# Kernel optimization log

Hardware: AMD Instinct MI355X
Metric: run time of the kernel (lower is better)

## Reference

```python
import jax, jax.numpy as jnp
import numpy as np

B, N, IN, OUT, H = 8, 256, 256, 256, 4
HD = OUT // H  # 64
ALPHA = 0.2    # LeakyReLU negative slope
EPS = 1e-5


def layernorm(x, g, b):
    m = x.mean(-1, keepdims=True)
    v = jnp.mean(jnp.square(x - m), axis=-1, keepdims=True)
    return (x - m) / jnp.sqrt(v + EPS) * g + b


def setup_inputs() -> dict:
    key = jax.random.key(0)
    ks = jax.random.split(key, 16)
    s = 0.05
    return {
        'h':    jax.random.normal(ks[0], (B, N, IN), jnp.float32),
        'adj':  jax.random.randint(ks[1], (B, N, N), 0, 2, jnp.int32),
        # per-head params (leading dim H)
        'W':    jax.random.normal(ks[2], (H, IN, HD), jnp.float32) * s,      # node proj (no bias)
        'We1':  jax.random.normal(ks[3], (H, 2 * IN, HD), jnp.float32) * s,  # edge_encoder lin
        'be1':  jnp.zeros((H, HD), jnp.float32),
        'Wa1':  jax.random.normal(ks[4], (H, 3 * HD, HD), jnp.float32) * s,  # attn mlp lin1
        'ba1':  jnp.zeros((H, HD), jnp.float32),
        'wa2':  jax.random.normal(ks[5], (H, HD), jnp.float32) * s,          # attn mlp lin2 -> scalar
        'ba2':  jnp.zeros((H,), jnp.float32),
        'ln_g': jnp.ones((H, HD), jnp.float32),   # per-head LayerNorm
        'ln_b': jnp.zeros((H, HD), jnp.float32),
        'Wo':   jax.random.normal(ks[6], (OUT, OUT), jnp.float32) * s,       # output projection
        'bo':   jnp.zeros((OUT,), jnp.float32),
        'ln2_g': jnp.ones((OUT,), jnp.float32),   # final LayerNorm
        'ln2_b': jnp.zeros((OUT,), jnp.float32),
    }


def _head(h, adj_mask, W, We1, be1, Wa1, ba1, wa2, ba2, g, b):
    # h: [B,N,IN]; adj_mask: [B,N,N] bool (True where adj==0)
    Wh = jnp.einsum('bnf,fd->bnd', h, W)                      # [B,N,HD]
    # attention MLP lin1 applied to concat([Wh_i, Wh_j, edge]):
    # split weight so the per-node parts are computed once, broadcast over pairs
    Wa, Wb, We = Wa1[:HD], Wa1[HD:2 * HD], Wa1[2 * HD:]
    si = jnp.einsum('bnd,de->bne', Wh, Wa) + ba1              # [B,N,HD]
    sj = jnp.einsum('bnd,de->bne', Wh, Wb)                    # [B,N,HD]
    # edge encoder: Linear(cat[h_i,h_j]) -> leaky_relu, split likewise
    ei = jnp.einsum('bnf,fd->bnd', h, We1[:IN]) + be1         # [B,N,HD]
    ej = jnp.einsum('bnf,fd->bnd', h, We1[IN:])               # [B,N,HD]
    edge = jax.nn.leaky_relu(ei[:, :, None, :] + ej[:, None, :, :], ALPHA)  # [B,N,N,HD]
    hidden = jax.nn.leaky_relu(
        si[:, :, None, :] + sj[:, None, :, :] + jnp.einsum('bijd,de->bije', edge, We),
        ALPHA)                                                # [B,N,N,HD]
    e = jnp.einsum('bijd,d->bij', hidden, wa2) + ba2          # [B,N,N]
    e = jnp.where(adj_mask, -1e9, e)
    attn = jax.nn.softmax(e, axis=-1)                         # [B,N,N]
    hp = jnp.einsum('bij,bjd->bid', attn, Wh)                 # [B,N,HD]
    return layernorm(hp, g, b)


def reference(h, adj, W, We1, be1, Wa1, ba1, wa2, ba2, ln_g, ln_b, Wo, bo, ln2_g, ln2_b):
    adj_mask = (adj == 0)
    heads = [
        _head(h, adj_mask, W[i], We1[i], be1[i], Wa1[i], ba1[i],
              wa2[i], ba2[i], ln_g[i], ln_b[i])
        for i in range(H)
    ]
    concat = jnp.concatenate(heads, axis=-1)                  # [B,N,OUT]
    out = jnp.einsum('bnf,fo->bno', concat, Wo) + bo
    out = out + h                                             # residual (IN == OUT)
    return layernorm(out, ln2_g, ln2_b)
```

## Files before the change

### kernel.cpp

```cpp
#include <hip/hip_runtime.h>
#include <hip/hip_bf16.h>

#define B_ 8
#define N_ 256
#define IN_ 256
#define OUT_ 256
#define H_ 4
#define HD_ 64
#define ALPHA_ 0.2f
#define EPS_ 1e-5f

#define S_ (B_*H_*N_*HD_)


typedef unsigned short ushort_t;
typedef __attribute__((ext_vector_type(8))) short short8;
typedef __attribute__((ext_vector_type(4))) float floatx4;

__device__ __forceinline__ float lrelu(float x) { return fmaxf(x, ALPHA_ * x); }
__device__ __forceinline__ ushort_t f2b(float x) {
    unsigned u = __float_as_uint(x);
    unsigned r = ((u >> 16) & 1u) + 0x7fffu;
    return (ushort_t)((u + r) >> 16);
}
__device__ __forceinline__ unsigned pk2(float x0, float x1) {
    __hip_bfloat162 p = __float22bfloat162_rn(make_float2(x0, x1));
    return *(unsigned*)&p;
}

__global__ __launch_bounds__(256) void setup_kernel(
    const float* __restrict__ h, const float* __restrict__ W,
    const float* __restrict__ We1, const float* __restrict__ Wa1,
    const float* __restrict__ Wo,
    ushort_t* __restrict__ h_b, ushort_t* __restrict__ wfull,
    ushort_t* __restrict__ wo_t, ushort_t* __restrict__ bw_b)
{
    const int blk = blockIdx.x;
    if (blk < 512) {
        const int i = (blk * 256 + threadIdx.x) * 4;
        float4 v = *(const float4*)&h[i];
        uint2 o; o.x = pk2(v.x, v.y); o.y = pk2(v.z, v.w);
        *(uint2*)&h_b[i] = o;
    } else if (blk < 1536) {
        const int bb = blk - 512;
        const int hh = bb >> 8, f = bb & 255;
        const int c = threadIdx.x;
        __shared__ float Wlds[64];
        if (c < 64) Wlds[c] = W[(size_t)(hh * 256 + f) * 64 + c];
        __syncthreads();
        float v;
        if (c < 64)       v = Wlds[c];
        else if (c < 128) v = We1[(size_t)(hh * 512 + f) * 64 + (c - 64)];
        else if (c < 192) v = We1[(size_t)(hh * 512 + 256 + f) * 64 + (c - 128)];
        else {
            float s = 0.f;
            const float* wa = Wa1 + (size_t)hh * 192 * 64 + (c - 192);
            #pragma unroll 4
            for (int g = 0; g < 64; ++g) s += Wlds[g] * wa[(size_t)g * 64];
            v = s;
        }
        wfull[(size_t)(hh * 256 + c) * 256 + f] = f2b(v);
    } else if (blk < 1552) {
        const int bb = blk - 1536;
        const int to = bb & 3, tf = bb >> 2;
        const int r0 = threadIdx.x >> 6, cc = threadIdx.x & 63;
        __shared__ float t[64][65];
        for (int rr = r0; rr < 64; rr += 4)
            t[rr][cc] = Wo[(size_t)(tf * 64 + rr) * 256 + to * 64 + cc];
        __syncthreads();
        for (int rr = r0; rr < 64; rr += 4)
            wo_t[(size_t)(to * 64 + rr) * 256 + tf * 64 + cc] = f2b(t[cc][rr]);
    } else {
        const int hh = blk - 1552;
        for (int idx = threadIdx.x; idx < 64 * 128; idx += 256) {
            const int e = idx >> 7, k = idx & 127;
            const int row = (k < 64) ? (128 + k) : k;
            bw_b[hh * 8192 + idx] = f2b(Wa1[(size_t)hh * 192 * 64 + row * 64 + e]);
        }
    }
}

__global__ __launch_bounds__(256) void prep2_kernel(
    const ushort_t* __restrict__ h_b, const ushort_t* __restrict__ wfull,
    const float* __restrict__ be1, const float* __restrict__ ba1,
    float* __restrict__ ws)
{
    const int gm = blockIdx.x & 63, gn = blockIdx.x >> 6;
    const int tid = threadIdx.x, lane = tid & 63, wid = tid >> 6;
    const int quad = lane >> 4, l15 = lane & 15;

    float*    ei_f = ws;
    float*    si_f = ws + S_;
    ushort_t* ej_b = (ushort_t*)(ws + 2 * (size_t)S_);
    ushort_t* Wh_b = ej_b + S_;
    ushort_t* WhT_b = (ushort_t*)(ws + 4 * (size_t)S_) + 262144 + 65536 + 32768;

    floatx4 acc[2][2];
    #pragma unroll
    for (int mt = 0; mt < 2; ++mt)
        #pragma unroll
        for (int nt = 0; nt < 2; ++nt) acc[mt][nt] = (floatx4){0.f,0.f,0.f,0.f};

    #pragma unroll 2
    for (int ks = 0; ks < 8; ++ks) {
        short8 afr[2], bfr[2];
        #pragma unroll
        for (int mt = 0; mt < 2; ++mt)
            afr[mt] = *(const short8*)&h_b[(size_t)(gm * 32 + mt * 16 + l15) * 256 + ks * 32 + quad * 8];
        #pragma unroll
        for (int nt = 0; nt < 2; ++nt)
            bfr[nt] = *(const short8*)&wfull[(size_t)(gn * 128 + wid * 32 + nt * 16 + l15) * 256 + ks * 32 + quad * 8];
        #pragma unroll
        for (int mt = 0; mt < 2; ++mt)
            #pragma unroll
            for (int nt = 0; nt < 2; ++nt)
                acc[mt][nt] = __builtin_amdgcn_mfma_f32_16x16x32_bf16(afr[mt], bfr[nt], acc[mt][nt], 0, 0, 0);
    }

    #pragma unroll
    for (int nt = 0; nt < 2; ++nt) {
        const int colg = gn * 128 + wid * 32 + nt * 16 + l15;
        const int head = colg >> 8, c = colg & 255, type = c >> 6, d = c & 63;
        #pragma unroll
        for (int mt = 0; mt < 2; ++mt)
            #pragma unroll
            for (int reg = 0; reg < 4; ++reg) {
                const int row = gm * 32 + mt * 16 + quad * 4 + reg;
                const int b = row >> 8, n = row & 255;
                const size_t idx = ((size_t)(b * H_ + head) * 256 + n) * 64 + d;
                const float v = acc[mt][nt][reg];
                if (type == 0) {
                    const ushort_t vb = f2b(v);
                    Wh_b[idx] = vb;
                    WhT_b[((size_t)(b * H_ + head) * 64 + d) * 256 + n] = vb;
                }
                else if (type == 1) ei_f[idx] = v + be1[head * 64 + d];
                else if (type == 2) ej_b[idx] = f2b(v);
                else                si_f[idx] = v + ba1[head * 64 + d];
            }
    }
}

__global__ __launch_bounds__(256, 2) void attn_kernel(
    const int* __restrict__ adj, const float* __restrict__ wa2,
    const float* __restrict__ ba2, const float* __restrict__ ln_g,
    const float* __restrict__ ln_b, float* __restrict__ ws)
{
    const int blk  = blockIdx.x;
    const int ig   = blk & 15;
    const int head = (blk >> 4) & 3;
    const int b    = blk >> 6;
    const int i0   = ig * 16;
    const int tid  = threadIdx.x;
    const int lane = tid & 63;
    const int wid  = tid >> 6;
    const int quad = lane >> 4;
    const int l15  = lane & 15;
    const int bh   = b * H_ + head;

    __shared__ float    P_s[16 * 256];
    __shared__ ushort_t Pb_s[16 * 264];
    __shared__ float    ei_s[16 * 64];
    __shared__ float    si_s[16 * 64];
    __shared__ unsigned long long adjm_s[16 * 4];
    __shared__ float    hp_s[16 * 68];

    const float*    ei_f = ws;
    const float*    si_f = ws + S_;
    const ushort_t* ej_b = (const ushort_t*)(ws + 2 * (size_t)S_);
    const ushort_t* Wh_b = ej_b + S_;
    ushort_t*       conc = (ushort_t*)(ws + 3 * (size_t)S_) + 524288;
    const ushort_t* bw_b = (const ushort_t*)(ws + 4 * (size_t)S_) + 262144 + 65536;
    const ushort_t* WhT_b = bw_b + 32768;

    {
        const int ii = tid >> 4, c = tid & 15;
        *(float4*)&ei_s[ii * 64 + c * 4] =
            *(const float4*)&ei_f[((size_t)(bh * 256 + i0 + ii)) * 64 + c * 4];
        *(float4*)&si_s[ii * 64 + c * 4] =
            *(const float4*)&si_f[((size_t)(bh * 256 + i0 + ii)) * 64 + c * 4];
    }
    {
        int av[16];
        #pragma unroll
        for (int r = 0; r < 16; ++r)
            av[r] = adj[((size_t)(b * 256 + i0 + r)) * 256 + tid];
        #pragma unroll
        for (int r = 0; r < 16; ++r) {
            unsigned long long mk = __ballot(av[r] != 0);
            if (lane == 0) adjm_s[r * 4 + wid] = mk;
        }
    }

    uint4  ejr[4][2];
    short8 bfrWe[4][2];
    floatx4 sjacc[4][4];
    #pragma unroll
    for (int mt = 0; mt < 4; ++mt) {
        const size_t jrow = (size_t)(bh * 256 + wid * 64 + mt * 16 + l15) * 64;
        #pragma unroll
        for (int kk = 0; kk < 2; ++kk)
            ejr[mt][kk] = *(const uint4*)&ej_b[jrow + kk * 32 + quad * 8];
    }
    #pragma unroll
    for (int nt = 0; nt < 4; ++nt)
        #pragma unroll
        for (int ks = 0; ks < 2; ++ks)
            bfrWe[nt][ks] = *(const short8*)&bw_b[head * 8192 + (nt * 16 + l15) * 128 + ks * 32 + quad * 8];
    {
        #pragma unroll
        for (int mt = 0; mt < 4; ++mt)
            #pragma unroll
            for (int nt = 0; nt < 4; ++nt) sjacc[mt][nt] = (floatx4){0.f,0.f,0.f,0.f};
        #pragma unroll
        for (int ks = 2; ks < 4; ++ks) {
            short8 whf[4], bfrWb[4];
            #pragma unroll
            for (int mt = 0; mt < 4; ++mt)
                whf[mt] = *(const short8*)&Wh_b[((size_t)(bh * 256 + wid * 64 + mt * 16 + l15)) * 64
                                                + (ks - 2) * 32 + quad * 8];
            #pragma unroll
            for (int nt = 0; nt < 4; ++nt)
                bfrWb[nt] = *(const short8*)&bw_b[head * 8192 + (nt * 16 + l15) * 128 + ks * 32 + quad * 8];
            #pragma unroll
            for (int mt = 0; mt < 4; ++mt)
                #pragma unroll
                for (int nt = 0; nt < 4; ++nt)
                    sjacc[mt][nt] = __builtin_amdgcn_mfma_f32_16x16x32_bf16(
                        whf[mt], bfrWb[nt], sjacc[mt][nt], 0, 0, 0);
        }
    }

    float wv[4];
    #pragma unroll
    for (int nt = 0; nt < 4; ++nt) wv[nt] = wa2[head * 64 + nt * 16 + l15];
    const float ba2h = ba2[head];

    __syncthreads();

    for (int i = 0; i < 16; ++i) {
        floatx4 acc[4][4];
        #pragma unroll
        for (int mt = 0; mt < 4; ++mt)
            #pragma unroll
            for (int nt = 0; nt < 4; ++nt) acc[mt][nt] = sjacc[mt][nt];

        #pragma unroll
        for (int ks = 0; ks < 2; ++ks) {
            short8 afr[4];
            float ev[8];
            *(float4*)&ev[0] = *(const float4*)&ei_s[i * 64 + ks * 32 + quad * 8];
            *(float4*)&ev[4] = *(const float4*)&ei_s[i * 64 + ks * 32 + quad * 8 + 4];
            #pragma unroll
            for (int mt = 0; mt < 4; ++mt) {
                const unsigned* rw = (const unsigned*)&ejr[mt][ks];
                union { unsigned u[4]; short8 s; } ow;
                #pragma unroll
                for (int p = 0; p < 4; ++p) {
                    float x0 = __uint_as_float(rw[p] << 16)         + ev[2 * p];
                    float x1 = __uint_as_float(rw[p] & 0xffff0000u) + ev[2 * p + 1];
                    ow.u[p] = pk2(lrelu(x0), lrelu(x1));
                }
                afr[mt] = ow.s;
            }
            #pragma unroll
            for (int mt = 0; mt < 4; ++mt)
                #pragma unroll
                for (int nt = 0; nt < 4; ++nt)
                    acc[mt][nt] = __builtin_amdgcn_mfma_f32_16x16x32_bf16(
                        afr[mt], bfrWe[nt][ks], acc[mt][nt], 0, 0, 0);
        }

        float sv[4];
        #pragma unroll
        for (int nt = 0; nt < 4; ++nt) sv[nt] = si_s[i * 64 + nt * 16 + l15];
        #pragma unroll
        for (int mt = 0; mt < 4; ++mt) {
            #pragma unroll
            for (int reg = 0; reg < 4; ++reg) {
                float val = 0.f;
                #pragma unroll
                for (int nt = 0; nt < 4; ++nt)
                    val += lrelu(acc[mt][nt][reg] + sv[nt]) * wv[nt];
                val += __shfl_xor(val, 1, 64);
                val += __shfl_xor(val, 2, 64);
                val += __shfl_xor(val, 4, 64);
                val += __shfl_xor(val, 8, 64);
                if (l15 == 0)
                    P_s[i * 256 + wid * 64 + mt * 16 + quad * 4 + reg] = val + ba2h;
            }
        }
    }
    __syncthreads();

    #pragma unroll
    for (int rr = 0; rr < 4; ++rr) {
        const int r = rr * 4 + wid;
        float4 v = *(const float4*)&P_s[r * 256 + lane * 4];
        const unsigned mk = (unsigned)(adjm_s[r * 4 + quad] >> (l15 * 4)) & 0xFu;
        float v0 = (mk & 1u) ? v.x : -1e9f;
        float v1 = (mk & 2u) ? v.y : -1e9f;
        float v2 = (mk & 4u) ? v.z : -1e9f;
        float v3 = (mk & 8u) ? v.w : -1e9f;
        float m = fmaxf(fmaxf(v0, v1), fmaxf(v2, v3));
        #pragma unroll
        for (int off = 32; off >= 1; off >>= 1) m = fmaxf(m, __shfl_xor(m, off, 64));
        float p0 = __expf(v0 - m), p1 = __expf(v1 - m);
        float p2 = __expf(v2 - m), p3 = __expf(v3 - m);
        float s = (p0 + p1) + (p2 + p3);
        #pragma unroll
        for (int off = 32; off >= 1; off >>= 1) s += __shfl_xor(s, off, 64);
        const float inv = 1.f / s;
        uint2 o; o.x = pk2(p0 * inv, p1 * inv); o.y = pk2(p2 * inv, p3 * inv);
        *(uint2*)&Pb_s[r * 264 + lane * 4] = o;
    }
    __syncthreads();

    floatx4 hacc = (floatx4){0.f,0.f,0.f,0.f};
    #pragma unroll
    for (int s = 0; s < 8; ++s) {
        short8 af = *(const short8*)&Pb_s[l15 * 264 + s * 32 + quad * 8];
        short8 bf = *(const short8*)&WhT_b[((size_t)(bh * 64) + wid * 16 + l15) * 256 + s * 32 + quad * 8];
        hacc = __builtin_amdgcn_mfma_f32_16x16x32_bf16(af, bf, hacc, 0, 0, 0);
    }
    #pragma unroll
    for (int reg = 0; reg < 4; ++reg)
        hp_s[(quad * 4 + reg) * 68 + wid * 16 + l15] = hacc[reg];
    __syncthreads();

    const float gg = ln_g[head * 64 + lane];
    const float bb = ln_b[head * 64 + lane];
    #pragma unroll
    for (int pss = 0; pss < 4; ++pss) {
        const int r = pss * 4 + wid;
        const float v = hp_s[r * 68 + lane];
        float s1 = v, s2 = v * v;
        #pragma unroll
        for (int off = 32; off >= 1; off >>= 1) {
            s1 += __shfl_xor(s1, off, 64);
            s2 += __shfl_xor(s2, off, 64);
        }
        const float mean = s1 * (1.f / 64.f);
        const float var = s2 * (1.f / 64.f) - mean * mean;
        const float o = (v - mean) * __frsqrt_rn(var + EPS_) * gg + bb;
        conc[((size_t)(b * 256 + i0 + r)) * 256 + head * 64 + lane] = f2b(o);
    }
}

__global__ __launch_bounds__(256) void out2_kernel(
    const float* __restrict__ h, const float* __restrict__ bo,
    const float* __restrict__ ln2_g, const float* __restrict__ ln2_b,
    const ushort_t* __restrict__ conc, const ushort_t* __restrict__ wo_t,
    float* __restrict__ out)
{
    const int rowbase = blockIdx.x * 16;
    const int tid = threadIdx.x, lane = tid & 63, wid = tid >> 6;
    const int quad = lane >> 4, l15 = lane & 15;

    __shared__ float s1a[16][4], s2a[16][4];

    floatx4 acc[4];
    #pragma unroll
    for (int nt = 0; nt < 4; ++nt) acc[nt] = (floatx4){0.f,0.f,0.f,0.f};

    #pragma unroll 2
    for (int ks = 0; ks < 8; ++ks) {
        short8 afr = *(const short8*)&conc[(size_t)(rowbase + l15) * 256 + ks * 32 + quad * 8];
        #pragma unroll
        for (int nt = 0; nt < 4; ++nt) {
            short8 bfr = *(const short8*)&wo_t[(size_t)(wid * 64 + nt * 16 + l15) * 256 + ks * 32 + quad * 8];
            acc[nt] = __builtin_amdgcn_mfma_f32_16x16x32_bf16(afr, bfr, acc[nt], 0, 0, 0);
        }
    }

    float x[4][4], s1[4], s2[4];
    #pragma unroll
    for (int reg = 0; reg < 4; ++reg) { s1[reg] = 0.f; s2[reg] = 0.f; }
    #pragma unroll
    for (int nt = 0; nt < 4; ++nt) {
        const int col = wid * 64 + nt * 16 + l15;
        const float bv = bo[col];
        #pragma unroll
        for (int reg = 0; reg < 4; ++reg) {
            const int row = rowbase + quad * 4 + reg;
            float v = acc[nt][reg] + bv + h[(size_t)row * 256 + col];
            x[nt][reg] = v;
            s1[reg] += v;
            s2[reg] += v * v;
        }
    }
    #pragma unroll
    for (int reg = 0; reg < 4; ++reg) {
        #pragma unroll
        for (int off = 1; off <= 8; off <<= 1) {
            s1[reg] += __shfl_xor(s1[reg], off, 64);
            s2[reg] += __shfl_xor(s2[reg], off, 64);
        }
        if (l15 == 0) {
            s1a[quad * 4 + reg][wid] = s1[reg];
            s2a[quad * 4 + reg][wid] = s2[reg];
        }
    }
    __syncthreads();

    #pragma unroll
    for (int reg = 0; reg < 4; ++reg) {
        const int r = quad * 4 + reg;
        const float S1 = s1a[r][0] + s1a[r][1] + s1a[r][2] + s1a[r][3];
        const float S2 = s2a[r][0] + s2a[r][1] + s2a[r][2] + s2a[r][3];
        const float mean = S1 * (1.f / 256.f);
        const float var = S2 * (1.f / 256.f) - mean * mean;
        const float rs = __frsqrt_rn(var + EPS_);
        const int row = rowbase + r;
        #pragma unroll
        for (int nt = 0; nt < 4; ++nt) {
            const int col = wid * 64 + nt * 16 + l15;
            out[(size_t)row * 256 + col] =
                (x[nt][reg] - mean) * rs * ln2_g[col] + ln2_b[col];
        }
    }
}

extern "C" void kernel_launch(void* const* d_in, const int* in_sizes, int n_in,
                              void* d_out, int out_size, void* d_ws, size_t ws_size,
                              hipStream_t stream)
{
    const float* h    = (const float*)d_in[0];
    const int*   adj  = (const int*)  d_in[1];
    const float* W    = (const float*)d_in[2];
    const float* We1  = (const float*)d_in[3];
    const float* be1  = (const float*)d_in[4];
    const float* Wa1  = (const float*)d_in[5];
    const float* ba1  = (const float*)d_in[6];
    const float* wa2  = (const float*)d_in[7];
    const float* ba2  = (const float*)d_in[8];
    const float* ln_g = (const float*)d_in[9];
    const float* ln_b = (const float*)d_in[10];
    const float* Wo   = (const float*)d_in[11];
    const float* bo   = (const float*)d_in[12];
    const float* ln2g = (const float*)d_in[13];
    const float* ln2b = (const float*)d_in[14];

    float* ws = (float*)d_ws;
    ushort_t* h_b   = (ushort_t*)(ws + 3 * (size_t)S_);
    ushort_t* conc  = h_b + 524288;
    ushort_t* wfull = (ushort_t*)(ws + 4 * (size_t)S_);
    ushort_t* wo_t  = wfull + 262144;
    ushort_t* bw_b  = wo_t + 65536;
    float* out = (float*)d_out;

    setup_kernel<<<1556, 256, 0, stream>>>(h, W, We1, Wa1, Wo, h_b, wfull, wo_t, bw_b);
    prep2_kernel<<<512,  256, 0, stream>>>(h_b, wfull, be1, ba1, ws);
    attn_kernel <<<512,  256, 0, stream>>>(adj, wa2, ba2, ln_g, ln_b, ws);
    out2_kernel <<<B_ * 16, 256, 0, stream>>>(h, bo, ln2g, ln2b, conc, wo_t, out);
}
```

Measured before the change: 187.8 us.

## Fuse h bf16 conversion into projection GEMM and restructure weight build kernel

The separate h-to-bf16 conversion pass is dropped; the projection GEMM now loads fp32 h directly and packs it to bf16 in registers. The weight-building kernel is reorganised from 1556 small blocks into 36 blocks that stage 64x64 tiles in shared memory, giving coalesced transposed writes to wfull. This removes one global round trip of h and many tiny blocks. In exchange, each GEMM block reads twice the bytes for the A operand and repeats the conversion, and the weight build runs on far fewer blocks.

```diff
diff --git a/kernel.cpp b/kernel.cpp
--- a/kernel.cpp
+++ b/kernel.cpp
@@ -28,42 +28,53 @@
     return *(unsigned*)&p;
 }
 
-__global__ __launch_bounds__(256) void setup_kernel(
-    const float* __restrict__ h, const float* __restrict__ W,
-    const float* __restrict__ We1, const float* __restrict__ Wa1,
-    const float* __restrict__ Wo,
-    ushort_t* __restrict__ h_b, ushort_t* __restrict__ wfull,
-    ushort_t* __restrict__ wo_t, ushort_t* __restrict__ bw_b)
+__global__ __launch_bounds__(256) void build_kernel(
+    const float* __restrict__ W, const float* __restrict__ We1,
+    const float* __restrict__ Wa1, const float* __restrict__ Wo,
+    ushort_t* __restrict__ wfull, ushort_t* __restrict__ wo_t,
+    ushort_t* __restrict__ bw_b)
 {
     const int blk = blockIdx.x;
-    if (blk < 512) {
-        const int i = (blk * 256 + threadIdx.x) * 4;
-        float4 v = *(const float4*)&h[i];
-        uint2 o; o.x = pk2(v.x, v.y); o.y = pk2(v.z, v.w);
-        *(uint2*)&h_b[i] = o;
-    } else if (blk < 1536) {
-        const int bb = blk - 512;
-        const int hh = bb >> 8, f = bb & 255;
-        const int c = threadIdx.x;
-        __shared__ float Wlds[64];
-        if (c < 64) Wlds[c] = W[(size_t)(hh * 256 + f) * 64 + c];
-        __syncthreads();
-        float v;
-        if (c < 64)       v = Wlds[c];
-        else if (c < 128) v = We1[(size_t)(hh * 512 + f) * 64 + (c - 64)];
-        else if (c < 192) v = We1[(size_t)(hh * 512 + 256 + f) * 64 + (c - 128)];
-        else {
-            float s = 0.f;
-            const float* wa = Wa1 + (size_t)hh * 192 * 64 + (c - 192);
-            #pragma unroll 4
-            for (int g = 0; g < 64; ++g) s += Wlds[g] * wa[(size_t)g * 64];
-            v = s;
-        }
-        wfull[(size_t)(hh * 256 + c) * 256 + f] = f2b(v);
-    } else if (blk < 1552) {
-        const int bb = blk - 1536;
+    const int tid = threadIdx.x;
+    if (blk < 16) {
+        const int hh = blk >> 2, cq = blk & 3;
+        __shared__ float tl[64][65];
+        __shared__ float wa_l[64][65];
+        const int r4 = tid >> 6;
+        const int cl = tid & 63;
+        if (cq == 3) {
+            for (int g = r4; g < 64; g += 4)
+                wa_l[g][cl] = Wa1[((size_t)hh * 192 + g) * 64 + cl];
+            __syncthreads();
+        }
+        for (int ft = 0; ft < 4; ++ft) {
+            const int f0 = ft * 64;
+            if (cq < 3) {
+                for (int r = r4; r < 64; r += 4) {
+                    float v;
+                    if (cq == 0)      v = W  [((size_t)hh * 256 + f0 + r) * 64 + cl];
+                    else if (cq == 1) v = We1[((size_t)hh * 512 + f0 + r) * 64 + cl];
+                    else              v = We1[((size_t)hh * 512 + 256 + f0 + r) * 64 + cl];
+                    tl[r][cl] = v;
+                }
+            } else {
+                for (int f = r4; f < 64; f += 4) {
+                    float acc = 0.f;
+                    const float* wrow = &W[((size_t)hh * 256 + f0 + f) * 64];
+                    #pragma unroll 8
+                    for (int g = 0; g < 64; ++g) acc += wrow[g] * wa_l[g][cl];
+                    tl[f][cl] = acc;
+                }
+            }
+            __syncthreads();
+            for (int cr = r4; cr < 64; cr += 4)
+                wfull[((size_t)hh * 256 + cq * 64 + cr) * 256 + f0 + cl] = f2b(tl[cl][cr]);
+            __syncthreads();
+        }
+    } else if (blk < 32) {
+        const int bb = blk - 16;
         const int to = bb & 3, tf = bb >> 2;
-        const int r0 = threadIdx.x >> 6, cc = threadIdx.x & 63;
+        const int r0 = tid >> 6, cc = tid & 63;
         __shared__ float t[64][65];
         for (int rr = r0; rr < 64; rr += 4)
             t[rr][cc] = Wo[(size_t)(tf * 64 + rr) * 256 + to * 64 + cc];
@@ -71,8 +82,8 @@
         for (int rr = r0; rr < 64; rr += 4)
             wo_t[(size_t)(to * 64 + rr) * 256 + tf * 64 + cc] = f2b(t[cc][rr]);
     } else {
-        const int hh = blk - 1552;
-        for (int idx = threadIdx.x; idx < 64 * 128; idx += 256) {
+        const int hh = blk - 32;
+        for (int idx = tid; idx < 64 * 128; idx += 256) {
             const int e = idx >> 7, k = idx & 127;
             const int row = (k < 64) ? (128 + k) : k;
             bw_b[hh * 8192 + idx] = f2b(Wa1[(size_t)hh * 192 * 64 + row * 64 + e]);
@@ -81,7 +92,7 @@
 }
 
 __global__ __launch_bounds__(256) void prep2_kernel(
-    const ushort_t* __restrict__ h_b, const ushort_t* __restrict__ wfull,
+    const float* __restrict__ h, const ushort_t* __restrict__ wfull,
     const float* __restrict__ be1, const float* __restrict__ ba1,
     float* __restrict__ ws)
 {
@@ -105,8 +116,15 @@
     for (int ks = 0; ks < 8; ++ks) {
         short8 afr[2], bfr[2];
         #pragma unroll
-        for (int mt = 0; mt < 2; ++mt)
-            afr[mt] = *(const short8*)&h_b[(size_t)(gm * 32 + mt * 16 + l15) * 256 + ks * 32 + quad * 8];
+        for (int mt = 0; mt < 2; ++mt) {
+            const float* hp0 = &h[(size_t)(gm * 32 + mt * 16 + l15) * 256 + ks * 32 + quad * 8];
+            float4 a0 = *(const float4*)hp0;
+            float4 a1 = *(const float4*)(hp0 + 4);
+            union { unsigned u[4]; short8 s; } aw;
+            aw.u[0] = pk2(a0.x, a0.y); aw.u[1] = pk2(a0.z, a0.w);
+            aw.u[2] = pk2(a1.x, a1.y); aw.u[3] = pk2(a1.z, a1.w);
+            afr[mt] = aw.s;
+        }
         #pragma unroll
         for (int nt = 0; nt < 2; ++nt)
             bfr[nt] = *(const short8*)&wfull[(size_t)(gn * 128 + wid * 32 + nt * 16 + l15) * 256 + ks * 32 + quad * 8];
@@ -442,15 +460,14 @@
     const float* ln2b = (const float*)d_in[14];
 
     float* ws = (float*)d_ws;
-    ushort_t* h_b   = (ushort_t*)(ws + 3 * (size_t)S_);
-    ushort_t* conc  = h_b + 524288;
+    ushort_t* conc  = (ushort_t*)(ws + 3 * (size_t)S_) + 524288;
     ushort_t* wfull = (ushort_t*)(ws + 4 * (size_t)S_);
     ushort_t* wo_t  = wfull + 262144;
     ushort_t* bw_b  = wo_t + 65536;
     float* out = (float*)d_out;
 
-    setup_kernel<<<1556, 256, 0, stream>>>(h, W, We1, Wa1, Wo, h_b, wfull, wo_t, bw_b);
-    prep2_kernel<<<512,  256, 0, stream>>>(h_b, wfull, be1, ba1, ws);
-    attn_kernel <<<512,  256, 0, stream>>>(adj, wa2, ba2, ln_g, ln_b, ws);
+    build_kernel<<<36,  256, 0, stream>>>(W, We1, Wa1, Wo, wfull, wo_t, bw_b);
+    prep2_kernel<<<512, 256, 0, stream>>>(h, wfull, be1, ba1, ws);
+    attn_kernel <<<512, 256, 0, stream>>>(adj, wa2, ba2, ln_g, ln_b, ws);
     out2_kernel <<<B_ * 16, 256, 0, stream>>>(h, bo, ln2g, ln2b, conc, wo_t, out);
 }
```

Measured after the change: 250.9 us. 33.6% more time.
